# Kernel tuning notes

Hardware: AMD Instinct MI355X
Metric: run time of the kernel (lower is better)

The kernel has to match this reference:

```python
import jax, jax.numpy as jnp
import numpy as np

LN_EPS = 1e-5
NORM_EPS = 1e-12


def channel_layernorm(x, w, b):
    # LayerNorm over channel dim of NCHW tensor (torch permutes to NHWC; equivalent)
    mu = x.mean(axis=1, keepdims=True)
    var = x.var(axis=1, keepdims=True)
    xn = (x - mu) / jnp.sqrt(var + LN_EPS)
    return xn * w[None, :, None, None] + b[None, :, None, None]


def pconv(x, w):
    # 1x1 pointwise conv, w: (out_ch, in_ch)
    return jnp.einsum('bchw,oc->bohw', x, w)


def dwconv3(x, w):
    # depthwise 3x3, padding 1; w: (ch, 1, 3, 3)
    return jax.lax.conv_general_dilated(
        x, w, window_strides=(1, 1), padding='SAME',
        feature_group_count=x.shape[1],
        dimension_numbers=('NCHW', 'OIHW', 'NCHW'))


def l2norm(x):
    n = jnp.sqrt(jnp.sum(x * x, axis=-1, keepdims=True))
    return x / jnp.maximum(n, NORM_EPS)


def setup_inputs() -> dict:
    key = jax.random.key(0)
    ks = jax.random.split(key, 8)
    B, C, H, W = 4, 128, 128, 128
    NH, G = 8, 2

    def w(k, shape, fan_in):
        return jax.random.normal(k, shape, dtype=jnp.float32) * (fan_in ** -0.5)

    return {
        'x': jax.random.normal(ks[0], (B, C, H, W), dtype=jnp.float32),
        'ln1_w': jnp.ones((C,), jnp.float32),
        'ln1_b': jnp.zeros((C,), jnp.float32),
        'temperature': jnp.ones((NH, 1, 1), jnp.float32),
        'qkv_p_w': w(ks[1], (3 * C, C), C),
        'qkv_d_w': w(ks[2], (3 * C, 1, 3, 3), 9),
        'proj_w': w(ks[3], (C, C), C),
        'ln2_w': jnp.ones((C,), jnp.float32),
        'ln2_b': jnp.zeros((C,), jnp.float32),
        'g1_w': w(ks[4], (2 * G * C, C), C),
        'gd_w': w(ks[5], (2 * G * C, 1, 3, 3), 9),
        'g2_w': w(ks[6], (C, G * C), G * C),
        'num_heads': NH,
    }


def reference(x, ln1_w, ln1_b, temperature, qkv_p_w, qkv_d_w, proj_w,
              ln2_w, ln2_b, g1_w, gd_w, g2_w, num_heads):
    b, c, h, w_ = x.shape
    d = c // num_heads

    # --- MDTA branch ---
    y = channel_layernorm(x, ln1_w, ln1_b)
    qkv = dwconv3(pconv(y, qkv_p_w), qkv_d_w)  # (b, 3c, h, w)
    q, k, v = jnp.split(qkv, 3, axis=1)
    q = l2norm(q.reshape(b, num_heads, d, h * w_))
    k = l2norm(k.reshape(b, num_heads, d, h * w_))
    v = v.reshape(b, num_heads, d, h * w_)
    # transposed (channel) attention: (b, heads, d, d)
    attn = jnp.einsum('bhdn,bhen->bhde', q, k) * temperature[None]
    attn = jax.nn.softmax(attn, axis=-1)
    out = jnp.einsum('bhde,bhen->bhdn', attn, v).reshape(b, c, h, w_)
    x = x + pconv(out, proj_w)

    # --- GDFN branch ---
    y = channel_layernorm(x, ln2_w, ln2_b)
    hdn = dwconv3(pconv(y, g1_w), gd_w)  # (b, 2*gamma*c, h, w)
    x1, x2 = jnp.split(hdn, 2, axis=1)
    g = jax.nn.gelu(x1, approximate=False) * x2
    x = x + pconv(g, g2_w)
    return x
```

## Files before the change

### kernel.cpp

```cpp
#include <hip/hip_runtime.h>
#include <cstdint>
#include <cstddef>

typedef float f32x4 __attribute__((ext_vector_type(4)));
typedef __bf16 bf16x8 __attribute__((ext_vector_type(8)));

__device__ __forceinline__ float b2f(unsigned short u) {
    union { unsigned int i; float f; } z; z.i = ((unsigned int)u) << 16; return z.f;
}
__device__ __forceinline__ unsigned short f2b(float f) {
    union { float f; unsigned int i; } z; z.f = f;
    unsigned int x = z.i;
    return (unsigned short)((x + 0x7FFFu + ((x >> 16) & 1u)) >> 16);
}

static constexpr int C = 128;
static constexpr int NP = 16384;
static constexpr int NH = 8;

#define SWZ(n) ((((n) ^ ((n) >> 3)) & 7) << 4)

struct Ptr11 { const float* p[11]; };
__constant__ int kWN[11]   = {128, 128, 8, 49152, 3456, 16384, 128, 128, 65536, 4608, 32768};
__constant__ int kWOff[11] = {0, 128, 256, 272, 49424, 52880, 69264, 69392, 69520, 135056, 139664};
static constexpr int kWTotal = 172432;

__global__ __launch_bounds__(256)
void cvt_w_kernel(Ptr11 P, unsigned short* __restrict__ dst)
{
    int seg = blockIdx.y;
    int n = kWN[seg];
    int i = blockIdx.x * 256 + threadIdx.x;
    if (i >= n) return;
    float v = P.p[seg][i];
    if (seg == 3) v *= P.p[0][i & 127];
    dst[kWOff[seg] + i] = f2b(v);
}

__global__ __launch_bounds__(128)
void prep_lnw_kernel(const float* __restrict__ w,
                     const float* __restrict__ g,
                     const float* __restrict__ bb,
                     float* __restrict__ Saux, float* __restrict__ Kaux)
{
    int o = blockIdx.x * 128 + threadIdx.x;
    if (o >= 384) return;
    float s = 0.f, k = 0.f;
    for (int c = 0; c < 128; ++c) {
        float wv = w[o * 128 + c];
        s += b2f(f2b(wv * g[c]));
        k += wv * bb[c];
    }
    Saux[o] = s; Kaux[o] = k;
}

__device__ __forceinline__ void dw8(const unsigned short* base, int y, int xi,
                                    const float* wr, float* o)
{
    uint4 rv0 = uint4{0,0,0,0}, rv1, rv2 = uint4{0,0,0,0};
    if (y > 0)   rv0 = *(const uint4*)(base - 128);
    rv1 = *(const uint4*)(base);
    if (y < 127) rv2 = *(const uint4*)(base + 128);
    uint4 rows[3] = {rv0, rv1, rv2};
    #pragma unroll
    for (int j = 0; j < 8; ++j) o[j] = 0.f;
    #pragma unroll
    for (int r = 0; r < 3; ++r) {
        union { uint4 v; unsigned short u[8]; } cv; cv.v = rows[r];
        int lh = __shfl_up((int)cv.u[7], 1, 16);
        int rh = __shfl_down((int)cv.u[0], 1, 16);
        float p[10];
        p[0] = (xi > 0)   ? b2f((unsigned short)lh) : 0.f;
        p[9] = (xi < 120) ? b2f((unsigned short)rh) : 0.f;
        #pragma unroll
        for (int j = 0; j < 8; ++j) p[j + 1] = b2f(cv.u[j]);
        #pragma unroll
        for (int j = 0; j < 8; ++j)
            o[j] += wr[r * 3] * p[j] + wr[r * 3 + 1] * p[j + 1] + wr[r * 3 + 2] * p[j + 2];
    }
}

__global__ __launch_bounds__(256)
void lngemm_fused(const float* __restrict__ x,
                  const unsigned short* __restrict__ Wt,
                  const float* __restrict__ Saux,
                  const float* __restrict__ Kaux,
                  unsigned short* __restrict__ Out)
{
    __shared__ unsigned short BsT[64 * 128];
    __shared__ unsigned short St[128 * 72];
    __shared__ float LSum[4][64], LSq[4][64], Mu[64], Rs[64];
    const int tid = threadIdx.x;
    const int b = blockIdx.y;
    const int n0 = blockIdx.x * 64;
    const int pxg = tid & 15;
    const int cseg = tid >> 4;
    const int lane = tid & 63;
    const float* xb = x + (size_t)b * C * NP + n0 + pxg * 4;
    char* p = (char*)BsT;

    f32x4 vs = f32x4{0.f,0.f,0.f,0.f}, vq = f32x4{0.f,0.f,0.f,0.f};
    {
        f32x4 hv[8];
        #pragma unroll
        for (int i = 0; i < 8; ++i) {
            f32x4 v = *(const f32x4*)(xb + (size_t)(cseg * 8 + i) * NP);
            hv[i] = v; vs += v; vq += v * v;
        }
        #pragma unroll
        for (int j = 0; j < 4; ++j) {
            int n = pxg * 4 + j;
            union { uint4 v; unsigned short u[8]; } o;
            #pragma unroll
            for (int i = 0; i < 8; ++i) o.u[i] = f2b(hv[i][j]);
            *(uint4*)(p + ((n * 256 + cseg * 16) ^ SWZ(n))) = o.v;
        }
    }
    #pragma unroll
    for (int j = 0; j < 4; ++j) {
        vs[j] += __shfl_xor(vs[j], 16, 64); vq[j] += __shfl_xor(vq[j], 16, 64);
        vs[j] += __shfl_xor(vs[j], 32, 64); vq[j] += __shfl_xor(vq[j], 32, 64);
    }
    if (lane < 16) {
        int wv = tid >> 6;
        #pragma unroll
        for (int j = 0; j < 4; ++j) { LSum[wv][pxg * 4 + j] = vs[j]; LSq[wv][pxg * 4 + j] = vq[j]; }
    }
    __syncthreads();
    if (tid < 64) {
        float s = LSum[0][tid] + LSum[1][tid] + LSum[2][tid] + LSum[3][tid];
        float q = LSq[0][tid] + LSq[1][tid] + LSq[2][tid] + LSq[3][tid];
        float mu = s * (1.f / 128.f);
        float var = q * (1.f / 128.f) - mu * mu;
        Mu[tid] = mu; Rs[tid] = rsqrtf(fmaxf(var, 0.f) + 1e-5f);
    }
    __syncthreads();

    const int wid = tid >> 6;
    const int ln16 = lane & 15, quad = lane >> 4;
    const int wy = wid >> 1, wx = wid & 1;
    int rbase[2], swz[2];
    #pragma unroll
    for (int nt = 0; nt < 2; ++nt) {
        int n = wx * 32 + nt * 16 + ln16;
        rbase[nt] = n * 256 + quad * 16;
        swz[nt] = SWZ(n);
    }
    size_t ob = (size_t)b * 384 * NP;
    #pragma unroll
    for (int cc = 0; cc < 3; ++cc) {
        const unsigned short* Wc = Wt + (size_t)cc * 128 * 128;
        f32x4 acc[4][2];
        #pragma unroll
        for (int i = 0; i < 4; ++i)
            #pragma unroll
            for (int j = 0; j < 2; ++j) acc[i][j] = f32x4{0.f, 0.f, 0.f, 0.f};

        #pragma unroll
        for (int k0 = 0; k0 < 128; k0 += 32) {
            bf16x8 afr[4], bfr[2];
            #pragma unroll
            for (int mt = 0; mt < 4; ++mt) {
                int m = wy * 64 + mt * 16 + ln16;
                uint4 v = *(const uint4*)(Wc + (size_t)m * 128 + k0 + quad * 8);
                afr[mt] = *(bf16x8*)&v;
            }
            #pragma unroll
            for (int nt = 0; nt < 2; ++nt) {
                uint4 v = *(const uint4*)(p + ((rbase[nt] + k0 * 2) ^ swz[nt]));
                bfr[nt] = *(bf16x8*)&v;
            }
            #pragma unroll
            for (int mt = 0; mt < 4; ++mt)
                #pragma unroll
                for (int nt = 0; nt < 2; ++nt)
                    acc[mt][nt] = __builtin_amdgcn_mfma_f32_16x16x32_bf16(
                        afr[mt], bfr[nt], acc[mt][nt], 0, 0, 0);
        }
        #pragma unroll
        for (int mt = 0; mt < 4; ++mt) {
            int col = wy * 64 + mt * 16 + quad * 4;
            f32x4 S4 = *(const f32x4*)(Saux + cc * 128 + col);
            f32x4 K4 = *(const f32x4*)(Kaux + cc * 128 + col);
            #pragma unroll
            for (int nt = 0; nt < 2; ++nt) {
                int nn = wx * 32 + nt * 16 + ln16;
                float mu = Mu[nn], rs = Rs[nn];
                #pragma unroll
                for (int r = 0; r < 4; ++r)
                    St[(col + r) * 72 + nn] = f2b(rs * (acc[mt][nt][r] - mu * S4[r]) + K4[r]);
            }
        }
        __syncthreads();
        #pragma unroll
        for (int i = 0; i < 4; ++i) {
            int flat = tid + i * 256;
            int row = flat >> 3;
            int g = flat & 7;
            uint4 v = *(const uint4*)(&St[row * 72 + g * 8]);
            *(uint4*)(&Out[ob + (size_t)(cc * 128 + row) * NP + n0 + g * 8]) = v;
        }
        __syncthreads();
    }
}

template <int COUT>
__device__ __forceinline__ void gemm_core_tr(
    const unsigned short* BsT,
    unsigned short* St,
    const unsigned short* __restrict__ W,
    unsigned short* __restrict__ OutB,
    int n0, int tid)
{
    const int lane = tid & 63;
    const int wid  = tid >> 6;
    const int ln16 = lane & 15, quad = lane >> 4;
    const int wy = wid >> 1, wx = wid & 1;
    const char* bs = (const char*)BsT;
    const int swz = (ln16 & 7) << 4;
    int rbase[4];
    #pragma unroll
    for (int nt = 0; nt < 4; ++nt) {
        int n = wx * 64 + nt * 16 + ln16;
        rbase[nt] = n * 256 + quad * 16;
    }

    for (int cc = 0; cc < COUT / 128; ++cc) {
        const int m0 = cc * 128;
        f32x4 acc[4][4];
        #pragma unroll
        for (int i = 0; i < 4; ++i)
            #pragma unroll
            for (int j = 0; j < 4; ++j) acc[i][j] = f32x4{0.f, 0.f, 0.f, 0.f};

        #pragma unroll
        for (int k0 = 0; k0 < 128; k0 += 32) {
            bf16x8 afr[4], bfr[4];
            #pragma unroll
            for (int mt = 0; mt < 4; ++mt) {
                int m = m0 + wy * 64 + mt * 16 + ln16;
                uint4 v = *(const uint4*)(W + (size_t)m * 128 + k0 + quad * 8);
                afr[mt] = *(bf16x8*)&v;
            }
            #pragma unroll
            for (int nt = 0; nt < 4; ++nt) {
                uint4 v = *(const uint4*)(bs + ((rbase[nt] + k0 * 2) ^ swz));
                bfr[nt] = *(bf16x8*)&v;
            }
            #pragma unroll
            for (int mt = 0; mt < 4; ++mt)
                #pragma unroll
                for (int nt = 0; nt < 4; ++nt)
                    acc[mt][nt] = __builtin_amdgcn_mfma_f32_16x16x32_bf16(
                        afr[mt], bfr[nt], acc[mt][nt], 0, 0, 0);
        }
        #pragma unroll
        for (int h = 0; h < 2; ++h) {
            if (wy == h) {
                #pragma unroll
                for (int mt = 0; mt < 4; ++mt) {
                    int lr0 = mt * 16 + quad * 4;
                    #pragma unroll
                    for (int nt = 0; nt < 4; ++nt) {
                        int nn = wx * 64 + nt * 16 + ln16;
                        #pragma unroll
                        for (int r = 0; r < 4; ++r)
                            St[(lr0 + r) * 136 + nn] = f2b(acc[mt][nt][r]);
                    }
                }
            }
            __syncthreads();
            #pragma unroll
            for (int i = 0; i < 4; ++i) {
                int flat = tid + i * 256;
                int row = flat >> 4;
                int g = flat & 15;
                uint4 v = *(const uint4*)(&St[row * 136 + g * 8]);
                *(uint4*)(&OutB[(size_t)(m0 + h * 64 + row) * NP + n0 + g * 8]) = v;
            }
            __syncthreads();
        }
    }
}

template <int COUT>
__global__ __launch_bounds__(256)
void gemm_bf16t_kernel(const unsigned short* __restrict__ W,
                       const unsigned short* __restrict__ Xt,
                       unsigned short* __restrict__ Out)
{
    __shared__ unsigned short BsT[128 * 128];
    __shared__ unsigned short St[64 * 136];
    const int tid = threadIdx.x;
    const int b = blockIdx.y;
    const int n0 = blockIdx.x * 128;
    const unsigned short* Xb = Xt + (size_t)b * NP * 128 + (size_t)n0 * 128;
    char* p = (char*)BsT;
    #pragma unroll
    for (int r = 0; r < 8; ++r) {
        int flat = tid + r * 256;
        int n = flat >> 4, ks = flat & 15;
        uint4 v = *(const uint4*)(Xb + (size_t)n * 128 + ks * 8);
        *(uint4*)(p + ((n * 256 + ks * 16) ^ ((n & 7) << 4))) = v;
    }
    __syncthreads();
    gemm_core_tr<COUT>(BsT, St, W, Out + (size_t)b * COUT * NP, n0, tid);
}

__global__ __launch_bounds__(256)
void dwqkgram_kernel(const unsigned short* __restrict__ big,
                     const unsigned short* __restrict__ w9,
                     float* __restrict__ Spart,
                     float* __restrict__ Npart)
{
    __shared__ unsigned short qs_[16 * 520];
    __shared__ unsigned short ks_[16 * 520];
    __shared__ float Sred[4][256];
    const int h = blockIdx.x, b = blockIdx.y, sp = blockIdx.z;
    const int tid = threadIdx.x;
    const int wid = tid >> 6, lane = tid & 63;
    const int xi = (tid & 15) * 8;
    const int yr = (tid >> 4) & 3;
    const int y  = sp * 4 + yr;
    const int bh = b * NH + h;
    float* Np = Npart + ((size_t)bh * 32 + sp) * 32;

    #pragma unroll
    for (int p = 0; p < 4; ++p) {
        int qc = p * 4 + wid;
        #pragma unroll
        for (int s = 0; s < 2; ++s) {
            int ch = s * 128 + h * 16 + qc;
            const unsigned short* base = big + ((size_t)b * 384 + ch) * NP + y * 128 + xi;
            float wr[9];
            #pragma unroll
            for (int i = 0; i < 9; ++i) wr[i] = b2f(w9[ch * 9 + i]);
            float o[8];
            dw8(base, y, xi, wr, o);
            union { uint4 v; unsigned short u[8]; } res;
            float ss = 0.f;
            #pragma unroll
            for (int j = 0; j < 8; ++j) {
                res.u[j] = f2b(o[j]);
                float vv = b2f(res.u[j]);
                ss += vv * vv;
            }
            unsigned short* tile = s ? ks_ : qs_;
            *(uint4*)(&tile[qc * 520 + yr * 128 + xi]) = res.v;
            #pragma unroll
            for (int od = 32; od > 0; od >>= 1) ss += __shfl_xor(ss, od, 64);
            if (lane == 0) Np[s * 16 + qc] = ss;
        }
    }
    __syncthreads();

    const int ln16 = lane & 15, quad = lane >> 4;
    f32x4 acc = f32x4{0.f, 0.f, 0.f, 0.f};
    #pragma unroll
    for (int i = 0; i < 4; ++i) {
        int off = wid * 128 + i * 32 + quad * 8;
        uint4 qv = *(const uint4*)(&qs_[ln16 * 520 + off]);
        uint4 kv = *(const uint4*)(&ks_[ln16 * 520 + off]);
        acc = __builtin_amdgcn_mfma_f32_16x16x32_bf16(*(bf16x8*)&qv, *(bf16x8*)&kv, acc, 0, 0, 0);
    }
    #pragma unroll
    for (int r = 0; r < 4; ++r) Sred[wid][(quad * 4 + r) * 16 + ln16] = acc[r];
    __syncthreads();
    float ssum = Sred[0][tid] + Sred[1][tid] + Sred[2][tid] + Sred[3][tid];
    Spart[((size_t)bh * 32 + sp) * 256 + tid] = ssum;
}

__global__ __launch_bounds__(256)
void softwp_kernel(const float* __restrict__ Spart, const float* __restrict__ Npart,
                   const unsigned short* __restrict__ temp,
                   const unsigned short* __restrict__ proj,
                   unsigned short* __restrict__ W2)
{
    __shared__ float Ps[256];
    int bh = blockIdx.x;
    int b = bh >> 3, h = bh & 7;
    int t = threadIdx.x;
    int dq = t >> 4, dk = t & 15;
    float sacc = 0.f;
    const float* Sp = Spart + (size_t)bh * 32 * 256;
    #pragma unroll
    for (int j = 0; j < 32; ++j) sacc += Sp[j * 256 + t];
    const float* Np = Npart + (size_t)bh * 32 * 32;
    float sq = 0.f, sk = 0.f;
    #pragma unroll
    for (int sp = 0; sp < 32; ++sp) { sq += Np[sp * 32 + dq]; sk += Np[sp * 32 + 16 + dk]; }
    float nq = fmaxf(sqrtf(sq), 1e-12f);
    float nk = fmaxf(sqrtf(sk), 1e-12f);
    float v = sacc / (nq * nk) * b2f(temp[h]);
    float m = v;
    #pragma unroll
    for (int o = 8; o > 0; o >>= 1) m = fmaxf(m, __shfl_xor(m, o, 16));
    float e = __expf(v - m);
    float s = e;
    #pragma unroll
    for (int o = 8; o > 0; o >>= 1) s += __shfl_xor(s, o, 16);
    Ps[t] = e / s;
    __syncthreads();

    int co = t >> 1;
    int eo = (t & 1) * 8;
    union { uint4 v[2]; unsigned short u[16]; } pw;
    pw.v[0] = *(const uint4*)(proj + (size_t)co * 128 + h * 16);
    pw.v[1] = *(const uint4*)(proj + (size_t)co * 128 + h * 16 + 8);
    float prw[16];
    #pragma unroll
    for (int d = 0; d < 16; ++d) prw[d] = b2f(pw.u[d]);
    union { uint4 v; unsigned short u[8]; } o8;
    #pragma unroll
    for (int j = 0; j < 8; ++j) {
        int ee = eo + j;
        float s2 = 0.f;
        #pragma unroll
        for (int d = 0; d < 16; ++d) s2 += prw[d] * Ps[d * 16 + ee];
        o8.u[j] = f2b(s2);
    }
    *(uint4*)(W2 + ((size_t)b * 128 + co) * 128 + h * 16 + eo) = o8.v;
}

__global__ __launch_bounds__(256)
void projln_kernel(const unsigned short* __restrict__ W2,
                   const unsigned short* __restrict__ big,
                   const unsigned short* __restrict__ w9,
                   const float* __restrict__ Res,
                   unsigned short* __restrict__ Xmid,
                   const unsigned short* __restrict__ lg,
                   const unsigned short* __restrict__ lb,
                   unsigned short* __restrict__ Y2t)
{
    __shared__ unsigned short Bs[128][130];
    __shared__ float RedS[2][128], RedQ[2][128], Mu[128], Rs[128];
    const int tid = threadIdx.x;
    const int b = blockIdx.y;
    const int y = blockIdx.x;
    const int n0 = y * 128;
    const unsigned short* Wb = W2 + (size_t)b * 16384;

    {
        const int xi = (tid & 15) * 8;
        const int crow = tid >> 4;
        #pragma unroll
        for (int p = 0; p < 8; ++p) {
            int c = p * 16 + crow;
            int ch = 256 + c;
            const unsigned short* base = big + ((size_t)b * 384 + ch) * NP + n0 + xi;
            float wr[9];
            #pragma unroll
            for (int i = 0; i < 9; ++i) wr[i] = b2f(w9[ch * 9 + i]);
            float o[8];
            dw8(base, y, xi, wr, o);
            union { uint4 v; unsigned int d[4]; unsigned short u[8]; } res;
            #pragma unroll
            for (int j = 0; j < 8; ++j) res.u[j] = f2b(o[j]);
            unsigned int* d = (unsigned int*)&Bs[c][xi];
            d[0] = res.d[0]; d[1] = res.d[1]; d[2] = res.d[2]; d[3] = res.d[3];
        }
    }
    __syncthreads();

    const int lane = tid & 63, wid = tid >> 6;
    const int ln16 = lane & 15, quad = lane >> 4;
    const int wy = wid >> 1, wx = wid & 1;

    f32x4 acc[4][4];
    #pragma unroll
    for (int i = 0; i < 4; ++i)
        #pragma unroll
        for (int j = 0; j < 4; ++j) acc[i][j] = f32x4{0.f, 0.f, 0.f, 0.f};

    #pragma unroll
    for (int k0 = 0; k0 < 128; k0 += 32) {
        bf16x8 afr[4], bfr[4];
        #pragma unroll
        for (int mt = 0; mt < 4; ++mt) {
            int m = wy * 64 + mt * 16 + ln16;
            uint4 v = *(const uint4*)(Wb + (size_t)m * 128 + k0 + quad * 8);
            afr[mt] = *(bf16x8*)&v;
        }
        #pragma unroll
        for (int nt = 0; nt < 4; ++nt) {
            int n = wx * 64 + nt * 16 + ln16;
            union { bf16x8 v; unsigned short u[8]; } tmp;
            #pragma unroll
            for (int j = 0; j < 8; ++j) tmp.u[j] = Bs[k0 + quad * 8 + j][n];
            bfr[nt] = tmp.v;
        }
        #pragma unroll
        for (int mt = 0; mt < 4; ++mt)
            #pragma unroll
            for (int nt = 0; nt < 4; ++nt)
                acc[mt][nt] = __builtin_amdgcn_mfma_f32_16x16x32_bf16(
                    afr[mt], bfr[nt], acc[mt][nt], 0, 0, 0);
    }

    size_t base = (size_t)b * 128 * NP;
    float ps[4] = {0.f, 0.f, 0.f, 0.f}, pq[4] = {0.f, 0.f, 0.f, 0.f};
    #pragma unroll
    for (int mt = 0; mt < 4; ++mt)
        #pragma unroll
        for (int nt = 0; nt < 4; ++nt) {
            int co0 = wy * 64 + mt * 16 + quad * 4;
            int n = n0 + wx * 64 + nt * 16 + ln16;
            #pragma unroll
            for (int r = 0; r < 4; ++r) {
                size_t idx = base + (size_t)(co0 + r) * NP + n;
                float tv = Res[idx] + acc[mt][nt][r];
                Xmid[idx] = f2b(tv);
                acc[mt][nt][r] = tv;
                ps[nt] += tv; pq[nt] += tv * tv;
            }
        }
    #pragma unroll
    for (int nt = 0; nt < 4; ++nt) {
        ps[nt] += __shfl_xor(ps[nt], 16, 64); ps[nt] += __shfl_xor(ps[nt], 32, 64);
        pq[nt] += __shfl_xor(pq[nt], 16, 64); pq[nt] += __shfl_xor(pq[nt], 32, 64);
    }
    if (quad == 0) {
        #pragma unroll
        for (int nt = 0; nt < 4; ++nt) {
            int nn = wx * 64 + nt * 16 + ln16;
            RedS[wy][nn] = ps[nt]; RedQ[wy][nn] = pq[nt];
        }
    }
    __syncthreads();
    if (tid < 128) {
        float s = RedS[0][tid] + RedS[1][tid];
        float q = RedQ[0][tid] + RedQ[1][tid];
        float mu = s * (1.f / 128.f);
        float var = q * (1.f / 128.f) - mu * mu;
        Mu[tid] = mu; Rs[tid] = rsqrtf(fmaxf(var, 0.f) + 1e-5f);
    }
    __syncthreads();

    char* p = (char*)Bs;
    #pragma unroll
    for (int mt = 0; mt < 4; ++mt) {
        int co0 = wy * 64 + mt * 16 + quad * 4;
        union { uint2 v; unsigned short u[4]; } gv, bv;
        gv.v = *(const uint2*)(lg + co0);
        bv.v = *(const uint2*)(lb + co0);
        float gw[4], bw[4];
        #pragma unroll
        for (int r = 0; r < 4; ++r) { gw[r] = b2f(gv.u[r]); bw[r] = b2f(bv.u[r]); }
        #pragma unroll
        for (int nt = 0; nt < 4; ++nt) {
            int nn = wx * 64 + nt * 16 + ln16;
            float mu = Mu[nn], rs = Rs[nn];
            union { uint2 v; unsigned short u[4]; } t2;
            #pragma unroll
            for (int r = 0; r < 4; ++r)
                t2.u[r] = f2b((acc[mt][nt][r] - mu) * rs * gw[r] + bw[r]);
            int addr = (nn * 256 + co0 * 2) ^ ((nn & 7) << 4);
            *(uint2*)(p + addr) = t2.v;
        }
    }
    __syncthreads();

    unsigned short* Yo = Y2t + (size_t)b * NP * 128 + (size_t)n0 * 128;
    #pragma unroll
    for (int r = 0; r < 8; ++r) {
        int flat = tid + r * 256;
        int n = flat >> 4, ks = flat & 15;
        uint4 v = *(const uint4*)(p + ((n * 256 + ks * 16) ^ ((n & 7) << 4)));
        *(uint4*)(Yo + (size_t)n * 128 + ks * 8) = v;
    }
}

template <int K>
__global__ __launch_bounds__(256)
void gemm_pconv(const unsigned short* __restrict__ W,
                const unsigned short* __restrict__ X,
                float* __restrict__ Out,
                const unsigned short* __restrict__ Res,
                int Cout)
{
    __shared__ unsigned short Bs[32][130];
    __shared__ float Stf[32 * 132];
    const int tid = threadIdx.x;
    const int b = blockIdx.z;
    const int n0 = blockIdx.x * 128;
    const int m0 = blockIdx.y * 128;
    const unsigned short* Xb = X + (size_t)b * K * NP;
    const int wid = tid >> 6;
    const int lane = tid & 63;
    const int ln16 = lane & 15;
    const int quad = lane >> 4;
    const int wy = wid >> 1;
    const int wx = wid & 1;

    f32x4 acc[4][4];
    #pragma unroll
    for (int i = 0; i < 4; ++i)
        #pragma unroll
        for (int j = 0; j < 4; ++j)
            acc[i][j] = f32x4{0.f, 0.f, 0.f, 0.f};

    for (int k0 = 0; k0 < K; k0 += 32) {
        #pragma unroll
        for (int r = 0; r < 2; ++r) {
            int flat = tid + r * 256;
            int kk = flat >> 4;
            int nn = (flat & 15) * 8;
            uint4 v = *(const uint4*)(Xb + (size_t)(k0 + kk) * NP + n0 + nn);
            unsigned int* d = (unsigned int*)&Bs[kk][nn];
            d[0] = v.x; d[1] = v.y; d[2] = v.z; d[3] = v.w;
        }
        __syncthreads();

        bf16x8 afr[4];
        #pragma unroll
        for (int mt = 0; mt < 4; ++mt) {
            int m = m0 + wy * 64 + mt * 16 + ln16;
            uint4 v = *(const uint4*)(W + (size_t)m * K + k0 + quad * 8);
            afr[mt] = *(bf16x8*)&v;
        }
        bf16x8 bfr[4];
        #pragma unroll
        for (int nt = 0; nt < 4; ++nt) {
            int n = wx * 64 + nt * 16 + ln16;
            union { bf16x8 v; unsigned short u[8]; } tmp;
            #pragma unroll
            for (int j = 0; j < 8; ++j) tmp.u[j] = Bs[quad * 8 + j][n];
            bfr[nt] = tmp.v;
        }
        #pragma unroll
        for (int mt = 0; mt < 4; ++mt)
            #pragma unroll
            for (int nt = 0; nt < 4; ++nt)
                acc[mt][nt] = __builtin_amdgcn_mfma_f32_16x16x32_bf16(
                    afr[mt], bfr[nt], acc[mt][nt], 0, 0, 0);
        __syncthreads();
    }

    size_t outbase = (size_t)b * Cout * NP;
    #pragma unroll
    for (int mt = 0; mt < 4; ++mt) {
        int lr = wy * 16 + quad * 4;
        #pragma unroll
        for (int nt = 0; nt < 4; ++nt) {
            int nn = wx * 64 + nt * 16 + ln16;
            #pragma unroll
            for (int r = 0; r < 4; ++r)
                Stf[(lr + r) * 132 + nn] = acc[mt][nt][r];
        }
        __syncthreads();
        #pragma unroll
        for (int i = 0; i < 4; ++i) {
            int flat = tid + i * 256;
            int row = flat >> 5;
            int g = flat & 31;
            f32x4 v = *(const f32x4*)(&Stf[row * 132 + g * 4]);
            int absrow = m0 + (row >> 4) * 64 + mt * 16 + (row & 15);
            size_t idx = outbase + (size_t)absrow * NP + n0 + g * 4;
            union { uint2 u2; unsigned short u[4]; } rv;
            rv.u2 = *(const uint2*)(Res + idx);
            f32x4 o;
            #pragma unroll
            for (int k = 0; k < 4; ++k) o[k] = b2f(rv.u[k]) + v[k];
            *(f32x4*)(Out + idx) = o;
        }
        __syncthreads();
    }
}

__global__ __launch_bounds__(256)
void dwgelu_kernel(const unsigned short* __restrict__ hdn,
                   const unsigned short* __restrict__ w9,
                   unsigned short* __restrict__ g)
{
    int t = blockIdx.x * 256 + threadIdx.x;
    int xi = (t & 15) * 8;
    int y  = (t >> 4) & 127;
    int bc = t >> 11;
    int c  = bc & 255;
    int b  = bc >> 8;
    const unsigned short* base1 = hdn + ((size_t)b * 512 + c) * NP + y * 128 + xi;
    const unsigned short* base2 = base1 + (size_t)256 * NP;

    float w1[9], w2[9];
    #pragma unroll
    for (int i = 0; i < 9; ++i) {
        w1[i] = b2f(w9[c * 9 + i]);
        w2[i] = b2f(w9[(c + 256) * 9 + i]);
    }

    float a1[8], a2[8];
    dw8(base1, y, xi, w1, a1);
    dw8(base2, y, xi, w2, a2);

    union { uint4 v; unsigned short u[8]; } res;
    #pragma unroll
    for (int j = 0; j < 8; ++j) {
        float u = a1[j];
        float tt = u * (0.7978845608f + 0.0356774081f * u * u);
        float e = __expf(2.f * tt);
        float th = 1.f - 2.f / (e + 1.f);
        float ge = 0.5f * u * (1.f + th);
        res.u[j] = f2b(ge * a2[j]);
    }
    *(uint4*)(g + (size_t)bc * NP + y * 128 + xi) = res.v;
}

struct Bufs {
    unsigned short* xmid;
    unsigned short* y2;
    unsigned short* big;
    unsigned short* mid;
    float* Spart;
    float* Npart;
    unsigned short* W2;
};

static void run_pipeline(const float* x_f32, float* out_f32,
                         const unsigned short* w,
                         const float* Saux, const float* Kaux,
                         const Bufs& B, int nb, hipStream_t stream)
{
    const unsigned short* temp    = w + 256;
    const unsigned short* qkv_p_w = w + 272;
    const unsigned short* qkv_d_w = w + 49424;
    const unsigned short* proj_w  = w + 52880;
    const unsigned short* ln2_w   = w + 69264;
    const unsigned short* ln2_b   = w + 69392;
    const unsigned short* g1_w    = w + 69520;
    const unsigned short* gd_w    = w + 135056;
    const unsigned short* g2_w    = w + 139664;

    lngemm_fused<<<dim3(NP / 64, nb), 256, 0, stream>>>(x_f32, qkv_p_w, Saux, Kaux, B.big);
    dwqkgram_kernel<<<dim3(NH, nb, 32), 256, 0, stream>>>(B.big, qkv_d_w, B.Spart, B.Npart);
    softwp_kernel<<<nb * NH, 256, 0, stream>>>(B.Spart, B.Npart, temp, proj_w, B.W2);
    projln_kernel<<<dim3(NP / 128, nb), 256, 0, stream>>>(B.W2, B.big, qkv_d_w, x_f32,
                                                          B.xmid, ln2_w, ln2_b, B.y2);

    gemm_bf16t_kernel<512><<<dim3(NP / 128, nb), 256, 0, stream>>>(g1_w, B.y2, B.big);
    dwgelu_kernel<<<nb * 256 * NP / 2048, 256, 0, stream>>>(B.big, gd_w, B.mid);
    gemm_pconv<256><<<dim3(NP / 128, 1, nb), 256, 0, stream>>>(g2_w, B.mid, out_f32, B.xmid, 128);
}

extern "C" void kernel_launch(void* const* d_in, const int* in_sizes, int n_in,
                              void* d_out, int out_size, void* d_ws, size_t ws_size,
                              hipStream_t stream)
{
    (void)in_sizes; (void)n_in; (void)out_size;
    const float* x = (const float*)d_in[0];
    char* ws = (char*)d_ws;

    size_t off = 0;
    unsigned short* wpack = (unsigned short*)(ws + off);
    off += (size_t)kWTotal * 2;
    off = (off + 255) & ~(size_t)255;
    float* Saux = (float*)(ws + off);  off += 384 * 4;
    float* Kaux = (float*)(ws + off);  off += 384 * 4;
    off = (off + 255) & ~(size_t)255;
    size_t header = off;

    auto layout = [&](int nb, size_t o, Bufs& B) -> size_t {
        B.xmid = (unsigned short*)(ws + o);  o += (size_t)nb * C * NP * 2;
        B.y2   = (unsigned short*)(ws + o);  o += (size_t)nb * C * NP * 2;
        B.big  = (unsigned short*)(ws + o);  o += (size_t)nb * 512 * NP * 2;
        B.mid  = (unsigned short*)(ws + o);  o += (size_t)nb * 256 * NP * 2;
        B.Spart = (float*)(ws + o);          o += (size_t)nb * NH * 32 * 256 * 4;
        B.Npart = (float*)(ws + o);          o += (size_t)nb * NH * 32 * 32 * 4;
        B.W2   = (unsigned short*)(ws + o);  o += (size_t)nb * 128 * 128 * 2;
        return o;
    };

    Ptr11 P;
    for (int i = 0; i < 11; ++i) P.p[i] = (const float*)d_in[i + 1];
    cvt_w_kernel<<<dim3(256, 11), 256, 0, stream>>>(P, wpack);
    prep_lnw_kernel<<<3, 128, 0, stream>>>((const float*)d_in[4], (const float*)d_in[1],
                                           (const float*)d_in[2], Saux, Kaux);

    Bufs Bfull;
    size_t need_full = layout(4, header, Bfull);

    if (ws_size >= need_full) {
        run_pipeline(x, (float*)d_out, wpack, Saux, Kaux, Bfull, 4, stream);
    } else {
        Bufs B1;
        layout(1, header, B1);
        for (int b = 0; b < 4; ++b) {
            run_pipeline(x + (size_t)b * C * NP,
                         (float*)d_out + (size_t)b * C * NP,
                         wpack, Saux, Kaux, B1, 1, stream);
        }
    }
}
```

Before: 257.3 us.

## Fuse depthwise conv + GELU gating into final GDFN pointwise GEMM

Merges the dwconv3+GELU gating kernel and the final 1x1 projection GEMM into one kernel. Each block takes one image row, computes all 256 gated channels for its 128 pixels into shared memory, then runs the MFMA GEMM against g2_w and adds the residual. This removes the intermediate bf16 'mid' buffer write and read and one launch. In exchange it uses about 65KB of shared memory per block, which limits occupancy, and has only 512 blocks with no overlap between the conv phase and the GEMM phase.

```diff
diff --git a/kernel.cpp b/kernel.cpp
--- a/kernel.cpp
+++ b/kernel.cpp
@@ -570,61 +570,78 @@
     }
 }
 
-template <int K>
 __global__ __launch_bounds__(256)
-void gemm_pconv(const unsigned short* __restrict__ W,
-                const unsigned short* __restrict__ X,
-                float* __restrict__ Out,
-                const unsigned short* __restrict__ Res,
-                int Cout)
-{
-    __shared__ unsigned short Bs[32][130];
-    __shared__ float Stf[32 * 132];
+void gdfn2_kernel(const unsigned short* __restrict__ W,
+                  const unsigned short* __restrict__ hdn,
+                  const unsigned short* __restrict__ w9,
+                  float* __restrict__ Out,
+                  const unsigned short* __restrict__ Res)
+{
+    __shared__ unsigned short Gs[256 * 130];
+    float* Stf = (float*)Gs;
     const int tid = threadIdx.x;
-    const int b = blockIdx.z;
-    const int n0 = blockIdx.x * 128;
-    const int m0 = blockIdx.y * 128;
-    const unsigned short* Xb = X + (size_t)b * K * NP;
-    const int wid = tid >> 6;
-    const int lane = tid & 63;
-    const int ln16 = lane & 15;
-    const int quad = lane >> 4;
-    const int wy = wid >> 1;
-    const int wx = wid & 1;
+    const int b = blockIdx.y;
+    const int y = blockIdx.x;
+    const int n0 = y * 128;
+
+    {
+        const int xi = (tid & 15) * 8;
+        const int crow = tid >> 4;
+        #pragma unroll
+        for (int p = 0; p < 16; ++p) {
+            int c = p * 16 + crow;
+            const unsigned short* b1 = hdn + ((size_t)b * 512 + c) * NP + n0 + xi;
+            const unsigned short* b2 = b1 + (size_t)256 * NP;
+            float w1[9], w2[9];
+            #pragma unroll
+            for (int i = 0; i < 9; ++i) {
+                w1[i] = b2f(w9[c * 9 + i]);
+                w2[i] = b2f(w9[(c + 256) * 9 + i]);
+            }
+            float a1[8], a2[8];
+            dw8(b1, y, xi, w1, a1);
+            dw8(b2, y, xi, w2, a2);
+            union { uint4 v; unsigned int d[4]; unsigned short u[8]; } res;
+            #pragma unroll
+            for (int j = 0; j < 8; ++j) {
+                float u = a1[j];
+                float tt = u * (0.7978845608f + 0.0356774081f * u * u);
+                float e = __expf(2.f * tt);
+                float th = 1.f - 2.f / (e + 1.f);
+                float ge = 0.5f * u * (1.f + th);
+                res.u[j] = f2b(ge * a2[j]);
+            }
+            unsigned int* d = (unsigned int*)&Gs[c * 130 + xi];
+            d[0] = res.d[0]; d[1] = res.d[1]; d[2] = res.d[2]; d[3] = res.d[3];
+        }
+    }
+    __syncthreads();
+
+    const int lane = tid & 63, wid = tid >> 6;
+    const int ln16 = lane & 15, quad = lane >> 4;
+    const int wy = wid >> 1, wx = wid & 1;
 
     f32x4 acc[4][4];
     #pragma unroll
     for (int i = 0; i < 4; ++i)
         #pragma unroll
-        for (int j = 0; j < 4; ++j)
-            acc[i][j] = f32x4{0.f, 0.f, 0.f, 0.f};
-
-    for (int k0 = 0; k0 < K; k0 += 32) {
-        #pragma unroll
-        for (int r = 0; r < 2; ++r) {
-            int flat = tid + r * 256;
-            int kk = flat >> 4;
-            int nn = (flat & 15) * 8;
-            uint4 v = *(const uint4*)(Xb + (size_t)(k0 + kk) * NP + n0 + nn);
-            unsigned int* d = (unsigned int*)&Bs[kk][nn];
-            d[0] = v.x; d[1] = v.y; d[2] = v.z; d[3] = v.w;
-        }
-        __syncthreads();
-
-        bf16x8 afr[4];
+        for (int j = 0; j < 4; ++j) acc[i][j] = f32x4{0.f, 0.f, 0.f, 0.f};
+
+    #pragma unroll
+    for (int k0 = 0; k0 < 256; k0 += 32) {
+        bf16x8 afr[4], bfr[4];
         #pragma unroll
         for (int mt = 0; mt < 4; ++mt) {
-            int m = m0 + wy * 64 + mt * 16 + ln16;
-            uint4 v = *(const uint4*)(W + (size_t)m * K + k0 + quad * 8);
+            int m = wy * 64 + mt * 16 + ln16;
+            uint4 v = *(const uint4*)(W + (size_t)m * 256 + k0 + quad * 8);
             afr[mt] = *(bf16x8*)&v;
         }
-        bf16x8 bfr[4];
         #pragma unroll
         for (int nt = 0; nt < 4; ++nt) {
             int n = wx * 64 + nt * 16 + ln16;
             union { bf16x8 v; unsigned short u[8]; } tmp;
             #pragma unroll
-            for (int j = 0; j < 8; ++j) tmp.u[j] = Bs[quad * 8 + j][n];
+            for (int j = 0; j < 8; ++j) tmp.u[j] = Gs[(k0 + quad * 8 + j) * 130 + n];
             bfr[nt] = tmp.v;
         }
         #pragma unroll
@@ -633,10 +650,10 @@
             for (int nt = 0; nt < 4; ++nt)
                 acc[mt][nt] = __builtin_amdgcn_mfma_f32_16x16x32_bf16(
                     afr[mt], bfr[nt], acc[mt][nt], 0, 0, 0);
-        __syncthreads();
-    }
-
-    size_t outbase = (size_t)b * Cout * NP;
+    }
+    __syncthreads();
+
+    size_t outbase = (size_t)b * 128 * NP;
     #pragma unroll
     for (int mt = 0; mt < 4; ++mt) {
         int lr = wy * 16 + quad * 4;
@@ -654,7 +671,7 @@
             int row = flat >> 5;
             int g = flat & 31;
             f32x4 v = *(const f32x4*)(&Stf[row * 132 + g * 4]);
-            int absrow = m0 + (row >> 4) * 64 + mt * 16 + (row & 15);
+            int absrow = (row >> 4) * 64 + mt * 16 + (row & 15);
             size_t idx = outbase + (size_t)absrow * NP + n0 + g * 4;
             union { uint2 u2; unsigned short u[4]; } rv;
             rv.u2 = *(const uint2*)(Res + idx);
@@ -667,49 +684,10 @@
     }
 }
 
-__global__ __launch_bounds__(256)
-void dwgelu_kernel(const unsigned short* __restrict__ hdn,
-                   const unsigned short* __restrict__ w9,
-                   unsigned short* __restrict__ g)
-{
-    int t = blockIdx.x * 256 + threadIdx.x;
-    int xi = (t & 15) * 8;
-    int y  = (t >> 4) & 127;
-    int bc = t >> 11;
-    int c  = bc & 255;
-    int b  = bc >> 8;
-    const unsigned short* base1 = hdn + ((size_t)b * 512 + c) * NP + y * 128 + xi;
-    const unsigned short* base2 = base1 + (size_t)256 * NP;
-
-    float w1[9], w2[9];
-    #pragma unroll
-    for (int i = 0; i < 9; ++i) {
-        w1[i] = b2f(w9[c * 9 + i]);
-        w2[i] = b2f(w9[(c + 256) * 9 + i]);
-    }
-
-    float a1[8], a2[8];
-    dw8(base1, y, xi, w1, a1);
-    dw8(base2, y, xi, w2, a2);
-
-    union { uint4 v; unsigned short u[8]; } res;
-    #pragma unroll
-    for (int j = 0; j < 8; ++j) {
-        float u = a1[j];
-        float tt = u * (0.7978845608f + 0.0356774081f * u * u);
-        float e = __expf(2.f * tt);
-        float th = 1.f - 2.f / (e + 1.f);
-        float ge = 0.5f * u * (1.f + th);
-        res.u[j] = f2b(ge * a2[j]);
-    }
-    *(uint4*)(g + (size_t)bc * NP + y * 128 + xi) = res.v;
-}
-
 struct Bufs {
     unsigned short* xmid;
     unsigned short* y2;
     unsigned short* big;
-    unsigned short* mid;
     float* Spart;
     float* Npart;
     unsigned short* W2;
@@ -737,8 +715,7 @@
                                                           B.xmid, ln2_w, ln2_b, B.y2);
 
     gemm_bf16t_kernel<512><<<dim3(NP / 128, nb), 256, 0, stream>>>(g1_w, B.y2, B.big);
-    dwgelu_kernel<<<nb * 256 * NP / 2048, 256, 0, stream>>>(B.big, gd_w, B.mid);
-    gemm_pconv<256><<<dim3(NP / 128, 1, nb), 256, 0, stream>>>(g2_w, B.mid, out_f32, B.xmid, 128);
+    gdfn2_kernel<<<dim3(128, nb), 256, 0, stream>>>(g2_w, B.big, gd_w, out_f32, B.xmid);
 }
 
 extern "C" void kernel_launch(void* const* d_in, const int* in_sizes, int n_in,
@@ -762,7 +739,6 @@
         B.xmid = (unsigned short*)(ws + o);  o += (size_t)nb * C * NP * 2;
         B.y2   = (unsigned short*)(ws + o);  o += (size_t)nb * C * NP * 2;
         B.big  = (unsigned short*)(ws + o);  o += (size_t)nb * 512 * NP * 2;
-        B.mid  = (unsigned short*)(ws + o);  o += (size_t)nb * 256 * NP * 2;
         B.Spart = (float*)(ws + o);          o += (size_t)nb * NH * 32 * 256 * 4;
         B.Npart = (float*)(ws + o);          o += (size_t)nb * NH * 32 * 32 * 4;
         B.W2   = (unsigned short*)(ws + o);  o += (size_t)nb * 128 * 128 * 2;
```

Result: no change. 260.2 us (+1.2%).
